# Kernel tuning notes

Hardware: AMD Instinct MI355X
Metric: run time of the kernel (lower is better)

The kernel has to match this reference:

```python
import jax, jax.numpy as jnp
import numpy as np

B, L, D = 2, 2048, 1024
H, G, Hd = 16, 4, 64
WIN = 256
HPG = H // G  # heads per group


def _sincos(seq_len, dim, dtype):
    # Matches sincos_cache: emb = cat(freqs, freqs) along last dim.
    inv_freq = 1.0 / (10000.0 ** (jnp.arange(0, dim, 2, dtype=jnp.float32) / dim))
    t = jnp.arange(seq_len, dtype=jnp.float32)
    freqs = t[:, None] * inv_freq[None, :]           # [L, dim/2]
    emb = jnp.concatenate([freqs, freqs], axis=-1)   # [L, dim]
    return jnp.sin(emb).astype(dtype), jnp.cos(emb).astype(dtype)


def _rope(x, sin, cos):
    # x: [B, h, L, Hd]; sin/cos: [L, Hd] broadcast over batch/heads.
    x1 = x[..., ::2]
    x2 = x[..., 1::2]
    xr = jnp.stack((-x2, x1), axis=-1).reshape(x.shape)  # interleaved rotate
    return x * cos[None, None] + xr * sin[None, None]


def setup_inputs() -> dict:
    key = jax.random.key(0)
    ks = jax.random.split(key, 10)
    s = 0.02
    return {
        "x": jax.random.normal(ks[0], (B, L, D), dtype=jnp.float32),
        "global_positions": jax.random.randint(ks[1], (4,), 0, L),
        "Wq": jax.random.normal(ks[2], (D, D), dtype=jnp.float32) * s,
        "bq": jnp.zeros((D,), dtype=jnp.float32),
        "Wk": jax.random.normal(ks[3], (D, G * Hd), dtype=jnp.float32) * s,
        "bk": jnp.zeros((G * Hd,), dtype=jnp.float32),
        "Wv": jax.random.normal(ks[4], (D, G * Hd), dtype=jnp.float32) * s,
        "bv": jnp.zeros((G * Hd,), dtype=jnp.float32),
        "Wo": jax.random.normal(ks[5], (D, D), dtype=jnp.float32) * s,
        "bo": jnp.zeros((D,), dtype=jnp.float32),
    }


def reference(x, global_positions, Wq, bq, Wk, bk, Wv, bv, Wo, bo):
    b, l, d = x.shape
    scale = 1.0 / np.sqrt(Hd).astype(np.float32)

    q = (x @ Wq + bq).reshape(b, l, H, Hd).transpose(0, 2, 1, 3)   # [B,H,L,Hd]
    k = (x @ Wk + bk).reshape(b, l, G, Hd).transpose(0, 2, 1, 3)   # [B,G,L,Hd]
    v = (x @ Wv + bv).reshape(b, l, G, Hd).transpose(0, 2, 1, 3)   # [B,G,L,Hd]

    sin, cos = _sincos(l, Hd, x.dtype)
    q = _rope(q, sin, cos)
    k = _rope(k, sin, cos)  # rope per-head is identical, so rope groups then expand

    # GQA broadcast: head h uses group h // HPG (group-major repeat)
    k = jnp.repeat(k, HPG, axis=1)  # [B,H,L,Hd]
    v = jnp.repeat(v, HPG, axis=1)  # [B,H,L,Hd]

    # sliding-window + global additive mask
    idx = jnp.arange(l)
    win = jnp.abs(idx[:, None] - idx[None, :]) <= WIN            # [L,L]
    isg = jnp.zeros((l,), dtype=bool).at[global_positions].set(True)
    mask = win | isg[:, None] | isg[None, :]
    addm = jnp.where(mask, 0.0, -jnp.inf).astype(x.dtype)        # [L,L]

    scores = jnp.einsum('bhld,bhsd->bhls', q, k) * scale + addm[None, None]
    probs = jax.nn.softmax(scores, axis=-1)
    out = jnp.einsum('bhls,bhsd->bhld', probs, v)                # [B,H,L,Hd]
    out = out.transpose(0, 2, 1, 3).reshape(b, l, d)
    return out @ Wo + bo
```

## Files before the change

kernel.cpp:

```cpp
#include <hip/hip_runtime.h>
#include <math.h>

#define B_   2
#define L_   2048
#define D_   1024
#define H_   16
#define G_   4
#define Hd_  64
#define WIN_ 256

typedef float f4 __attribute__((ext_vector_type(4)));
typedef float f32x4 __attribute__((ext_vector_type(4)));
typedef short s16x8 __attribute__((ext_vector_type(8)));
typedef ushort u16x4 __attribute__((ext_vector_type(4)));

#define ROPE_LN 0.28782313662425575

__device__ __forceinline__ float bf2f(ushort u) {
    union { uint i; float f; } c; c.i = ((uint)u) << 16; return c.f;
}
__device__ __forceinline__ ushort f2bf(float f) {
    union { float f; uint i; } c; c.f = f;
    return (ushort)((c.i + 0x7FFFu + ((c.i >> 16) & 1u)) >> 16);
}
__device__ __forceinline__ uint cvtpk(float lo, float hi) {
    uint r;
    asm("v_cvt_pk_bf16_f32 %0, %1, %2" : "=v"(r) : "v"(lo), "v"(hi));
    return r;
}

__device__ __forceinline__ void async_copy16(const ushort* g, ushort* l) {
    __builtin_amdgcn_global_load_lds(
        (const __attribute__((address_space(1))) void*)g,
        (__attribute__((address_space(3))) void*)l,
        16, 0, 0);
}

__global__ __launch_bounds__(256) void k_prep_all(
    const float* __restrict__ x, ushort* __restrict__ xb,
    const float* __restrict__ Wq, const float* __restrict__ Wk,
    const float* __restrict__ Wv, const float* __restrict__ Wo,
    ushort* __restrict__ Wt, ushort* __restrict__ Wot,
    float* __restrict__ sct)
{
    __shared__ __align__(16) float Ts[64][68];
    const int bid = blockIdx.x;
    const int tid = threadIdx.x;

    if (bid < 4096) {
        const int idx = bid * 256 + tid;
        f4 v = ((const f4*)x)[idx];
        u16x4 o;
        o[0] = f2bf(v[0]); o[1] = f2bf(v[1]); o[2] = f2bf(v[2]); o[3] = f2bf(v[3]);
        ((u16x4*)xb)[idx] = o;
        return;
    }
    if (bid >= 5120) {
        const int idx = (bid - 5120) * 256 + tid;
        const int l = idx >> 5, m = idx & 31;
        const float invf = (float)exp(-ROPE_LN * (double)m);
        const float a = (float)l * invf;
        sct[l * 64 + m]      = cosf(a);
        sct[l * 64 + 32 + m] = sinf(a);
        return;
    }
    const int t = bid - 4096;
    const int z = t >> 8;
    const float* W; ushort* dst; int N, rowoff;
    if (z == 0)      { W = Wq; N = 1024; dst = Wt;  rowoff = 0;    }
    else if (z == 1) { W = Wk; N = 256;  dst = Wt;  rowoff = 1024; }
    else if (z == 2) { W = Wv; N = 256;  dst = Wt;  rowoff = 1280; }
    else             { W = Wo; N = 1024; dst = Wot; rowoff = 0;    }
    const int k0 = ((t >> 4) & 15) << 6;
    const int n0 = (t & 15) << 6;
    if (n0 >= N) return;
    const int rr = tid >> 4, cc4 = (tid & 15) << 2;
#pragma unroll
    for (int i = 0; i < 4; ++i) {
        const int r = rr + i * 16;
        *(f4*)&Ts[r][cc4] = *(const f4*)&W[(size_t)(k0 + r) * N + n0 + cc4];
    }
    __syncthreads();
#pragma unroll
    for (int i = 0; i < 4; ++i) {
        const int tr = rr + i * 16;
        u16x4 pk;
#pragma unroll
        for (int j = 0; j < 4; ++j) pk[j] = f2bf(Ts[cc4 + j][tr]);
        *(u16x4*)&dst[(size_t)(rowoff + n0 + tr) * 1024 + k0 + cc4] = pk;
    }
}

__global__ __launch_bounds__(256) void k_gemm_bf16(
    const ushort* __restrict__ A, const ushort* __restrict__ Bt, int mode,
    const float* __restrict__ b0, const float* __restrict__ b1,
    const float* __restrict__ b2, const float* __restrict__ sct,
    ushort* __restrict__ qo, ushort* __restrict__ ko, ushort* __restrict__ vt,
    float* __restrict__ outp)
{
    __shared__ __align__(16) ushort LDSbuf[16384];
    ushort* As = LDSbuf;
    ushort* Bs = LDSbuf + 8192;

    const int tid = threadIdx.x;
    const int wv = tid >> 6, lane = tid & 63, lr = lane & 15, lg = lane >> 4;
    const int wm = wv >> 1, wn = wv & 1;
    const int rblk = blockIdx.x << 7, cblk = blockIdx.y << 6;

    const ushort* agp[4]; ushort* alds[4];
#pragma unroll
    for (int i = 0; i < 4; ++i) {
        const int slot = wv * 256 + i * 64 + lane;
        const int r = slot >> 3, c = slot & 7;
        const int ss = c ^ (r & 7);
        agp[i] = A + (size_t)(rblk + r) * 1024 + ss * 8;
        alds[i] = As + (wv * 256 + i * 64) * 8;
    }
    const ushort* bgp[2]; ushort* blds[2];
#pragma unroll
    for (int i = 0; i < 2; ++i) {
        const int slot = wv * 128 + i * 64 + lane;
        const int r = slot >> 3, c = slot & 7;
        const int ss = c ^ (r & 7);
        bgp[i] = Bt + (size_t)(cblk + r) * 1024 + ss * 8;
        blds[i] = Bs + (wv * 128 + i * 64) * 8;
    }

    f32x4 acc[4][2];
#pragma unroll
    for (int m = 0; m < 4; ++m)
#pragma unroll
        for (int n = 0; n < 2; ++n) acc[m][n] = (f32x4)0.f;

    for (int kt = 0; kt < 16; ++kt) {
        if (kt) __syncthreads();
        const int ko_ = kt * 64;
#pragma unroll
        for (int i = 0; i < 4; ++i) async_copy16(agp[i] + ko_, alds[i]);
#pragma unroll
        for (int i = 0; i < 2; ++i) async_copy16(bgp[i] + ko_, blds[i]);
        __syncthreads();

#pragma unroll
        for (int ks = 0; ks < 2; ++ks) {
            s16x8 aF[4], bF[2];
#pragma unroll
            for (int m = 0; m < 4; ++m) {
                const int r = wm * 64 + m * 16 + lr;
                const int c = (ks * 4 + lg) ^ (r & 7);
                aF[m] = *(const s16x8*)&As[r * 64 + c * 8];
            }
#pragma unroll
            for (int n = 0; n < 2; ++n) {
                const int r = wn * 32 + n * 16 + lr;
                const int c = (ks * 4 + lg) ^ (r & 7);
                bF[n] = *(const s16x8*)&Bs[r * 64 + c * 8];
            }
            __builtin_amdgcn_s_setprio(1);
#pragma unroll
            for (int m = 0; m < 4; ++m)
#pragma unroll
                for (int n = 0; n < 2; ++n)
                    acc[m][n] = __builtin_amdgcn_mfma_f32_16x16x32_bf16(aF[m], bF[n], acc[m][n], 0, 0, 0);
            __builtin_amdgcn_s_setprio(0);
        }
    }

    if (mode == 0) {
        const bool dorope = (cblk < 1280);
        float* tab = (float*)LDSbuf;
        if (dorope) {
            __syncthreads();
            const float* srcT = sct + (size_t)(rblk & 2047) * 64;
            for (int i = tid; i < 2048; i += 256)
                ((f4*)tab)[i] = ((const f4*)srcT)[i];
            __syncthreads();
        }
#pragma unroll
        for (int m = 0; m < 4; ++m) {
            const int row0 = rblk + wm * 64 + m * 16 + (lg << 2);
            const int bb = row0 >> 11, l0 = row0 & 2047;
            const int ll0 = row0 - rblk;
#pragma unroll
            for (int n = 0; n < 2; ++n) {
                const int col = cblk + wn * 32 + n * 16 + lr;
                float v_[4];
                const float bi = (col < 1024) ? b0[col]
                               : (col < 1280) ? b1[col - 1024] : b2[col - 1280];
#pragma unroll
                for (int rg = 0; rg < 4; ++rg) v_[rg] = acc[m][n][rg] + bi;
                if (dorope) {
                    const int mI = col & 31;
                    const float sgn = (lr & 1) ? 1.f : -1.f;
#pragma unroll
                    for (int rg = 0; rg < 4; ++rg) {
                        const float part = __shfl_xor(v_[rg], 1);
                        const float c_ = tab[(ll0 + rg) * 64 + mI];
                        const float s_ = tab[(ll0 + rg) * 64 + 32 + mI];
                        v_[rg] = v_[rg] * c_ + sgn * part * s_;
                    }
                }
                if (col < 1024) {
                    const int h = col >> 6, d = col & 63;
                    ushort* p = qo + (((size_t)(bb * 16 + h)) * 2048 + l0) * 64 + d;
#pragma unroll
                    for (int rg = 0; rg < 4; ++rg)
                        p[(size_t)rg * 64] = f2bf(v_[rg] * 0.125f);
                } else if (col < 1280) {
                    const int cl = col - 1024, g = cl >> 6, d = cl & 63;
                    ushort* p = ko + (((size_t)(bb * 4 + g)) * 2048 + l0) * 64 + d;
#pragma unroll
                    for (int rg = 0; rg < 4; ++rg)
                        p[(size_t)rg * 64] = f2bf(v_[rg]);
                } else {
                    const int cl = col - 1280, g = cl >> 6, d = cl & 63;
                    u16x4 pk;
#pragma unroll
                    for (int rg = 0; rg < 4; ++rg) pk[rg] = f2bf(v_[rg]);
                    *(u16x4*)(vt + ((size_t)(bb * 4 + g) * 64 + d) * 2048 + l0) = pk;
                }
            }
        }
    } else {
#pragma unroll
        for (int m = 0; m < 4; ++m) {
            const int row0 = rblk + wm * 64 + m * 16 + (lg << 2);
#pragma unroll
            for (int n = 0; n < 2; ++n) {
                const int col = cblk + wn * 32 + n * 16 + lr;
                const float bi = b0[col];
#pragma unroll
                for (int rg = 0; rg < 4; ++rg)
                    outp[(size_t)(row0 + rg) * 1024 + col] = acc[m][n][rg] + bi;
            }
        }
    }
}

__global__ __launch_bounds__(256, 4) void k_attn_win(
    const ushort* __restrict__ qb, const ushort* __restrict__ kb,
    const ushort* __restrict__ vtb, const int* __restrict__ gpos,
    ushort* __restrict__ aout)
{
    __shared__ __align__(16) ushort Ks[2][4096];
    __shared__ __align__(16) ushort Vs[2][4096];
    __shared__ ushort Pl[4][1024];

    const int tid  = threadIdx.x;
    const int wv   = tid >> 6, lane = tid & 63;
    const int lr   = lane & 15, lg = lane >> 4;
    const int qt = blockIdx.x, g = blockIdx.y, b = blockIdx.z;
    const int h  = (g << 2) + wv;
    const int q0w = qt << 4;
    const int qpos = q0w + lr;

    const ushort* qp = qb  + (((size_t)b * H_ + h) * L_ + q0w) * Hd_;
    const ushort* kp = kb  + ((size_t)b * G_ + g) * (size_t)L_ * Hd_;
    const ushort* vp = vtb + ((size_t)b * G_ + g) * (size_t)Hd_ * L_;
    char* rowp = (char*)&Pl[wv][0] + (lr << 7);
    const int swz = (lr & 7) << 4;

    int sr[2], ssk[2];
    ushort* kl[2]; ushort* vl[2];
#pragma unroll
    for (int i = 0; i < 2; ++i) {
        const int slot = wv * 128 + i * 64 + lane;
        const int r = slot >> 3, c = slot & 7;
        sr[i] = r; ssk[i] = c ^ (r & 7);
        kl[i] = ((ushort*)Ks) + (wv * 128 + i * 64) * 8;
        vl[i] = ((ushort*)Vs) + (wv * 128 + i * 64) * 8;
    }

#define STAGE(CUR, S0_) do {                                                  \
    _Pragma("unroll") for (int i = 0; i < 2; ++i) {                           \
        async_copy16(kp + ((size_t)(S0_) + sr[i]) * 64 + ssk[i] * 8,          \
                     kl[i] + (CUR) * 4096);                                   \
        async_copy16(vp + (size_t)sr[i] * 2048 + (S0_) + ssk[i] * 8,          \
                     vl[i] + (CUR) * 4096);                                   \
    } } while (0)

    const s16x8* qr = (const s16x8*)(qp + (size_t)lr * Hd_);
    const s16x8 qf0 = qr[lg], qf1 = qr[lg + 4];

    int gall[4];
#pragma unroll
    for (int j = 0; j < 4; ++j) gall[j] = gpos[j];
    bool uniq[4];
    uniq[0] = true;
    uniq[1] = (gall[1] != gall[0]);
    uniq[2] = (gall[2] != gall[0]) && (gall[2] != gall[1]);
    uniq[3] = (gall[3] != gall[0]) && (gall[3] != gall[1]) && (gall[3] != gall[2]);

    f32x4 acc_o[4];
#pragma unroll
    for (int j = 0; j < 4; ++j) acc_o[j] = (f32x4)0.f;
    float mrun = -INFINITY, lrun = 0.f;

    const int t_lo = (q0w - WIN_ > 0) ? ((q0w - WIN_) >> 6) : 0;
    const int t_hi_f = (q0w + 15 + WIN_) >> 6;
    const int t_hi = (t_hi_f < (L_ >> 6) - 1) ? t_hi_f : (L_ >> 6) - 1;

    const int kc0 = lg ^ (lr & 7);
    const int kc1 = (lg + 4) ^ (lr & 7);

    int cur = 0;
    STAGE(0, t_lo << 6);

    for (int t = t_lo; t <= t_hi; ++t) {
        const int s0 = t << 6;
        __syncthreads();
        if (t < t_hi) STAGE(cur ^ 1, (t + 1) << 6);

        const ushort* Kb = ((const ushort*)Ks) + cur * 4096;
        const ushort* Vb = ((const ushort*)Vs) + cur * 4096;

        f32x4 s[4];
#pragma unroll
        for (int gk = 0; gk < 4; ++gk) {
            const int gr = gk * 16 + lr;
            s16x8 kf0 = *(const s16x8*)&Kb[(gr * 8 + kc0) * 8];
            s16x8 kf1 = *(const s16x8*)&Kb[(gr * 8 + kc1) * 8];
            f32x4 tq = __builtin_amdgcn_mfma_f32_16x16x32_bf16(kf0, qf0, (f32x4)0.f, 0, 0, 0);
            s[gk]    = __builtin_amdgcn_mfma_f32_16x16x32_bf16(kf1, qf1, tq, 0, 0, 0);
        }

        s16x8 vf0[4], vf1[4];
#pragma unroll
        for (int dg = 0; dg < 4; ++dg) {
            const int vrw = dg * 16 + lr;
            vf0[dg] = *(const s16x8*)&Vb[(vrw * 8 + kc0) * 8];
            vf1[dg] = *(const s16x8*)&Vb[(vrw * 8 + kc1) * 8];
        }

        if (s0 < q0w - 241 || s0 > q0w + 193) {
#pragma unroll
            for (int gk = 0; gk < 4; ++gk)
#pragma unroll
                for (int r2 = 0; r2 < 4; ++r2) {
                    const int key = s0 + gk * 16 + (lg << 2) + r2;
                    const int dlt = qpos - key;
                    if (dlt > WIN_ || dlt < -WIN_) s[gk][r2] = -INFINITY;
                }
        }

        float mx = fmaxf(fmaxf(s[0][0], s[0][1]), fmaxf(s[0][2], s[0][3]));
#pragma unroll
        for (int gk = 1; gk < 4; ++gk)
            mx = fmaxf(mx, fmaxf(fmaxf(s[gk][0], s[gk][1]), fmaxf(s[gk][2], s[gk][3])));
        mx = fmaxf(mx, __shfl_xor(mx, 16));
        mx = fmaxf(mx, __shfl_xor(mx, 32));
        const float mn = fmaxf(mrun, mx);
        const float al = __expf(mrun - mn);

        float rs = 0.f;
        uint pk0[4], pk1[4];
#pragma unroll
        for (int gk = 0; gk < 4; ++gk) {
            const float p0 = __expf(s[gk][0] - mn);
            const float p1 = __expf(s[gk][1] - mn);
            const float p2 = __expf(s[gk][2] - mn);
            const float p3 = __expf(s[gk][3] - mn);
            rs += (p0 + p1) + (p2 + p3);
            pk0[gk] = cvtpk(p0, p1);
            pk1[gk] = cvtpk(p2, p3);
        }
        rs += __shfl_xor(rs, 16);
        rs += __shfl_xor(rs, 32);
        lrun = lrun * al + rs;
        mrun = mn;

#pragma unroll
        for (int gk = 0; gk < 4; ++gk) {
            uint2 w; w.x = pk0[gk]; w.y = pk1[gk];
            *(uint2*)(rowp + (((gk << 5) + (lg << 3)) ^ swz)) = w;
        }

        f32x4 al4;
#pragma unroll
        for (int r = 0; r < 4; ++r)
            al4[r] = __shfl(al, (lane & 48) + (lg << 2) + r);
#pragma unroll
        for (int j = 0; j < 4; ++j) acc_o[j] *= al4;

        const s16x8 pa0 = *(const s16x8*)(rowp + ((lg << 4) ^ swz));
        const s16x8 pa1 = *(const s16x8*)(rowp + ((64 + (lg << 4)) ^ swz));
        __builtin_amdgcn_s_setprio(1);
#pragma unroll
        for (int dg = 0; dg < 4; ++dg) {
            acc_o[dg] = __builtin_amdgcn_mfma_f32_16x16x32_bf16(pa0, vf0[dg], acc_o[dg], 0, 0, 0);
            acc_o[dg] = __builtin_amdgcn_mfma_f32_16x16x32_bf16(pa1, vf1[dg], acc_o[dg], 0, 0, 0);
        }
        __builtin_amdgcn_s_setprio(0);

        cur ^= 1;
    }

    {
        const s16x8* kr = (const s16x8*)(kp + (size_t)gall[lr & 3] * 64);
        s16x8 kf0 = kr[lg], kf1 = kr[lg + 4];
        f32x4 tq = __builtin_amdgcn_mfma_f32_16x16x32_bf16(kf0, qf0, (f32x4)0.f, 0, 0, 0);
        f32x4 sv = __builtin_amdgcn_mfma_f32_16x16x32_bf16(kf1, qf1, tq, 0, 0, 0);

#pragma unroll
        for (int r2 = 0; r2 < 4; ++r2) {
            bool valid = (lg == 0) && uniq[r2];
            const int dlt = qpos - gall[r2];
            valid = valid && ((dlt > WIN_) || (dlt < -WIN_));
            if (!valid) sv[r2] = -INFINITY;
        }

        float mx = fmaxf(fmaxf(sv[0], sv[1]), fmaxf(sv[2], sv[3]));
        mx = fmaxf(mx, __shfl_xor(mx, 16));
        mx = fmaxf(mx, __shfl_xor(mx, 32));
        const float mn = fmaxf(mrun, mx);
        const float al = __expf(mrun - mn);
        const float p0 = __expf(sv[0] - mn);
        const float p1 = __expf(sv[1] - mn);
        const float p2 = __expf(sv[2] - mn);
        const float p3 = __expf(sv[3] - mn);
        float rs = (p0 + p1) + (p2 + p3);
        rs += __shfl_xor(rs, 16);
        rs += __shfl_xor(rs, 32);
        lrun = lrun * al + rs;
        mrun = mn;

        uint2 w; w.x = cvtpk(p0, p1); w.y = cvtpk(p2, p3);
        *(uint2*)(rowp + ((lg << 3) ^ swz)) = w;
        uint2 z; z.x = 0; z.y = 0;
        *(uint2*)(rowp + ((32 + (lg << 3)) ^ swz)) = z;

        f32x4 al4;
#pragma unroll
        for (int r = 0; r < 4; ++r)
            al4[r] = __shfl(al, (lane & 48) + (lg << 2) + r);
#pragma unroll
        for (int j = 0; j < 4; ++j) acc_o[j] *= al4;

        const s16x8 pa0 = *(const s16x8*)(rowp + ((lg << 4) ^ swz));
#pragma unroll
        for (int dg = 0; dg < 4; ++dg) {
            s16x8 vb0 = (s16x8)(short)0;
            if (lg == 0) {
#pragma unroll
                for (int j = 0; j < 4; ++j)
                    vb0[j] = (short)vp[(size_t)(dg * 16 + lr) * 2048 + gall[j]];
            }
            acc_o[dg] = __builtin_amdgcn_mfma_f32_16x16x32_bf16(pa0, vb0, acc_o[dg], 0, 0, 0);
        }
    }

    {
        const float inv = 1.f / lrun;
#pragma unroll
        for (int r = 0; r < 4; ++r) {
            const float w0 = __shfl(inv, (lane & 48) + (lg << 2) + r);
            const int qrow = q0w + (lg << 2) + r;
            ushort* op = aout + (((size_t)b * L_ + qrow) * H_ + h) * Hd_;
#pragma unroll
            for (int dg = 0; dg < 4; ++dg)
                op[dg * 16 + lr] = f2bf(acc_o[dg][r] * w0);
        }
    }
#undef STAGE
}

__global__ __launch_bounds__(256) void k_attn_global_rows(
    const ushort* __restrict__ q, const ushort* __restrict__ kg,
    const ushort* __restrict__ vt, const int* __restrict__ gpos,
    ushort* __restrict__ aout)
{
    __shared__ float qrow[64];
    __shared__ float Ps[L_];
    __shared__ float red[4];
    __shared__ float pacc[4][64];

    const int tid = threadIdx.x;
    const int wv = tid >> 6, lane = tid & 63;
    const int b = blockIdx.x >> 4;
    const int h = blockIdx.x & 15;
    const int g = h >> 2;
    const int gi = blockIdx.y;
    const int lq = gpos[gi];
    for (int j = 0; j < gi; ++j)
        if (gpos[j] == lq) return;
    const ushort* kbase = kg + ((size_t)b * G_ + g) * (size_t)L_ * Hd_;
    const ushort* vbase = vt + ((size_t)b * G_ + g) * (size_t)Hd_ * L_;

    if (tid < 64) qrow[tid] = bf2f(q[(((size_t)b * H_ + h) * L_ + lq) * Hd_ + tid]);
    __syncthreads();

    float sc[8]; float lmax = -INFINITY;
#pragma unroll
    for (int c = 0; c < 8; ++c) {
        const int s = tid + (c << 8);
        const s16x8* kr = (const s16x8*)(kbase + (size_t)s * Hd_);
        float dot = 0.f;
#pragma unroll
        for (int d8 = 0; d8 < 8; ++d8) {
            s16x8 kv = kr[d8];
#pragma unroll
            for (int j = 0; j < 8; ++j) dot += qrow[d8 * 8 + j] * bf2f((ushort)kv[j]);
        }
        sc[c] = dot; lmax = fmaxf(lmax, dot);
    }
#pragma unroll
    for (int o = 32; o; o >>= 1) lmax = fmaxf(lmax, __shfl_xor(lmax, o));
    if (lane == 0) red[wv] = lmax;
    __syncthreads();
    const float M = fmaxf(fmaxf(red[0], red[1]), fmaxf(red[2], red[3]));
    __syncthreads();

    float ls = 0.f;
#pragma unroll
    for (int c = 0; c < 8; ++c) {
        const float p = __expf(sc[c] - M);
        Ps[tid + (c << 8)] = p;
        ls += p;
    }
#pragma unroll
    for (int o = 32; o; o >>= 1) ls += __shfl_xor(ls, o);
    if (lane == 0) red[wv] = ls;
    __syncthreads();
    const float S = red[0] + red[1] + red[2] + red[3];

    const int d = tid & 63, ch = tid >> 6;
    const ushort* vr = vbase + (size_t)d * L_ + (ch << 9);
    float a = 0.f;
    for (int s8 = 0; s8 < 64; ++s8) {
        s16x8 vv = ((const s16x8*)vr)[s8];
        const float* pp = &Ps[(ch << 9) + (s8 << 3)];
#pragma unroll
        for (int j = 0; j < 8; ++j) a += pp[j] * bf2f((ushort)vv[j]);
    }
    pacc[ch][d] = a;
    __syncthreads();
    if (tid < 64) {
        const float sum = pacc[0][tid] + pacc[1][tid] + pacc[2][tid] + pacc[3][tid];
        aout[(((size_t)b * L_ + lq) * H_ + h) * Hd_ + tid] = f2bf(sum / S);
    }
}

extern "C" void kernel_launch(void* const* d_in, const int* in_sizes, int n_in,
                              void* d_out, int out_size, void* d_ws, size_t ws_size,
                              hipStream_t stream)
{
    const float* x  = (const float*)d_in[0];
    const int*   gp = (const int*)d_in[1];
    const float* Wq = (const float*)d_in[2];
    const float* bq = (const float*)d_in[3];
    const float* Wk = (const float*)d_in[4];
    const float* bk = (const float*)d_in[5];
    const float* Wv = (const float*)d_in[6];
    const float* bv = (const float*)d_in[7];
    const float* Wo = (const float*)d_in[8];
    const float* bo = (const float*)d_in[9];
    float* out = (float*)d_out;

    ushort* xb   = (ushort*)d_ws;
    ushort* awsb = xb;
    ushort* qws  = xb  + (size_t)4194304;
    ushort* kws  = qws + (size_t)4194304;
    ushort* vtws = kws + (size_t)1048576;
    ushort* Wt   = vtws + (size_t)1048576;
    ushort* Wot  = Wt  + (size_t)1572864;
    float*  sct  = (float*)(Wot + (size_t)1048576);

    k_prep_all<<<dim3(5376), 256, 0, stream>>>(x, xb, Wq, Wk, Wv, Wo, Wt, Wot, sct);

    k_gemm_bf16<<<dim3(32, 24), 256, 0, stream>>>(xb, Wt, 0, bq, bk, bv, sct,
                                                  qws, kws, vtws, (float*)0);

    k_attn_win<<<dim3(128, 4, 2), 256, 0, stream>>>(qws, kws, vtws, gp, awsb);
    k_attn_global_rows<<<dim3(32, 4), 256, 0, stream>>>(qws, kws, vtws, gp, awsb);

    k_gemm_bf16<<<dim3(32, 16), 256, 0, stream>>>(awsb, Wot, 1, bo, (const float*)0,
                                                  (const float*)0, (const float*)0,
                                                  (ushort*)0, (ushort*)0, (ushort*)0, out);
}
```

Baseline: 104.2 us.

## Process two 16-row query subtiles per wave to reuse staged K/V tiles

Each attention block now covers 32 query rows instead of 16, with each wave keeping two independent online-softmax states and accumulators. Every K/V tile loaded into shared memory is used by both sub-tiles, roughly halving K/V global traffic and staging per query row, and the grid shrinks to half as many blocks. In exchange register pressure rises (launch bounds lowered from 4 to 3 blocks per CU), each block walks one extra key tile, and there are fewer blocks to fill the GPU.

```diff
diff --git a/kernel.cpp b/kernel.cpp
--- a/kernel.cpp
+++ b/kernel.cpp
@@ -237,7 +237,119 @@
     }
 }
 
-__global__ __launch_bounds__(256, 4) void k_attn_win(
+#define PROCSUB(Q0S, QF0, QF1, MRUN, LRUN, ACC) do {                          \
+    f32x4 s_[4];                                                              \
+    _Pragma("unroll") for (int gk = 0; gk < 4; ++gk) {                        \
+        const int gr_ = gk * 16 + lr;                                         \
+        s16x8 kf0_ = *(const s16x8*)&Kb[(gr_ * 8 + kc0) * 8];                 \
+        s16x8 kf1_ = *(const s16x8*)&Kb[(gr_ * 8 + kc1) * 8];                 \
+        f32x4 tq_ = __builtin_amdgcn_mfma_f32_16x16x32_bf16(kf0_, QF0, (f32x4)0.f, 0, 0, 0); \
+        s_[gk]    = __builtin_amdgcn_mfma_f32_16x16x32_bf16(kf1_, QF1, tq_, 0, 0, 0); \
+    }                                                                         \
+    if (s0 < (Q0S) - 241 || s0 > (Q0S) + 193) {                               \
+        _Pragma("unroll") for (int gk = 0; gk < 4; ++gk)                      \
+        _Pragma("unroll") for (int r2 = 0; r2 < 4; ++r2) {                    \
+            const int key_ = s0 + gk * 16 + (lg << 2) + r2;                   \
+            const int dlt_ = ((Q0S) + lr) - key_;                             \
+            if (dlt_ > WIN_ || dlt_ < -WIN_) s_[gk][r2] = -INFINITY;          \
+        }                                                                     \
+    }                                                                         \
+    float mx_ = fmaxf(fmaxf(s_[0][0], s_[0][1]), fmaxf(s_[0][2], s_[0][3]));  \
+    _Pragma("unroll") for (int gk = 1; gk < 4; ++gk)                          \
+        mx_ = fmaxf(mx_, fmaxf(fmaxf(s_[gk][0], s_[gk][1]), fmaxf(s_[gk][2], s_[gk][3]))); \
+    mx_ = fmaxf(mx_, __shfl_xor(mx_, 16));                                    \
+    mx_ = fmaxf(mx_, __shfl_xor(mx_, 32));                                    \
+    const float mn_ = fmaxf(MRUN, mx_);                                       \
+    const float al_ = __expf(MRUN - mn_);                \
+    float rs_ = 0.f;                                                          \
+    uint pk0_[4], pk1_[4];                                                    \
+    _Pragma("unroll") for (int gk = 0; gk < 4; ++gk) {                        \
+        const float p0_ = __expf(s_[gk][0] - mn_);                            \
+        const float p1_ = __expf(s_[gk][1] - mn_);                            \
+        const float p2_ = __expf(s_[gk][2] - mn_);                            \
+        const float p3_ = __expf(s_[gk][3] - mn_);                            \
+        rs_ += (p0_ + p1_) + (p2_ + p3_);                                     \
+        pk0_[gk] = cvtpk(p0_, p1_);                                           \
+        pk1_[gk] = cvtpk(p2_, p3_);                                           \
+    }                                                                         \
+    rs_ += __shfl_xor(rs_, 16);                                               \
+    rs_ += __shfl_xor(rs_, 32);                                               \
+    LRUN = LRUN * al_ + rs_;                                                  \
+    MRUN = mn_;                                                               \
+    _Pragma("unroll") for (int gk = 0; gk < 4; ++gk) {                        \
+        uint2 w_; w_.x = pk0_[gk]; w_.y = pk1_[gk];                           \
+        *(uint2*)(rowp + (((gk << 5) + (lg << 3)) ^ swz)) = w_;               \
+    }                                                                         \
+    f32x4 al4_;                                                               \
+    _Pragma("unroll") for (int r = 0; r < 4; ++r)                             \
+        al4_[r] = __shfl(al_, (lane & 48) + (lg << 2) + r);                   \
+    _Pragma("unroll") for (int j = 0; j < 4; ++j) ACC[j] *= al4_;             \
+    const s16x8 pa0_ = *(const s16x8*)(rowp + ((lg << 4) ^ swz));             \
+    const s16x8 pa1_ = *(const s16x8*)(rowp + ((64 + (lg << 4)) ^ swz));      \
+    __builtin_amdgcn_s_setprio(1);                                            \
+    _Pragma("unroll") for (int dg = 0; dg < 4; ++dg) {                        \
+        ACC[dg] = __builtin_amdgcn_mfma_f32_16x16x32_bf16(pa0_, vf0[dg], ACC[dg], 0, 0, 0); \
+        ACC[dg] = __builtin_amdgcn_mfma_f32_16x16x32_bf16(pa1_, vf1[dg], ACC[dg], 0, 0, 0); \
+    }                                                                         \
+    __builtin_amdgcn_s_setprio(0);                                            \
+} while (0)
+
+#define PSEUDO(Q0S, QF0, QF1, MRUN, LRUN, ACC) do {                           \
+    const s16x8* kr_ = (const s16x8*)(kp + (size_t)gall[lr & 3] * 64);        \
+    s16x8 kf0_ = kr_[lg], kf1_ = kr_[lg + 4];                                 \
+    f32x4 tq_ = __builtin_amdgcn_mfma_f32_16x16x32_bf16(kf0_, QF0, (f32x4)0.f, 0, 0, 0); \
+    f32x4 sv_ = __builtin_amdgcn_mfma_f32_16x16x32_bf16(kf1_, QF1, tq_, 0, 0, 0); \
+    _Pragma("unroll") for (int r2 = 0; r2 < 4; ++r2) {                        \
+        bool valid_ = (lg == 0) && uniq[r2];                                  \
+        const int dlt_ = ((Q0S) + lr) - gall[r2];                             \
+        valid_ = valid_ && ((dlt_ > WIN_) || (dlt_ < -WIN_));                 \
+        if (!valid_) sv_[r2] = -INFINITY;                                     \
+    }                                                                         \
+    float mx_ = fmaxf(fmaxf(sv_[0], sv_[1]), fmaxf(sv_[2], sv_[3]));          \
+    mx_ = fmaxf(mx_, __shfl_xor(mx_, 16));                                    \
+    mx_ = fmaxf(mx_, __shfl_xor(mx_, 32));                                    \
+    const float mn_ = fmaxf(MRUN, mx_);                                       \
+    const float al_ = __expf(MRUN - mn_);                                     \
+    const float p0_ = __expf(sv_[0] - mn_);                                   \
+    const float p1_ = __expf(sv_[1] - mn_);                                   \
+    const float p2_ = __expf(sv_[2] - mn_);                                   \
+    const float p3_ = __expf(sv_[3] - mn_);                                   \
+    float rs_ = (p0_ + p1_) + (p2_ + p3_);                                    \
+    rs_ += __shfl_xor(rs_, 16);                                               \
+    rs_ += __shfl_xor(rs_, 32);                                               \
+    LRUN = LRUN * al_ + rs_;                                                  \
+    MRUN = mn_;                                                               \
+    uint2 w_; w_.x = cvtpk(p0_, p1_); w_.y = cvtpk(p2_, p3_);                 \
+    *(uint2*)(rowp + ((lg << 3) ^ swz)) = w_;                                 \
+    uint2 z_; z_.x = 0; z_.y = 0;                                             \
+    *(uint2*)(rowp + ((32 + (lg << 3)) ^ swz)) = z_;                          \
+    f32x4 al4_;                                                               \
+    _Pragma("unroll") for (int r = 0; r < 4; ++r)                             \
+        al4_[r] = __shfl(al_, (lane & 48) + (lg << 2) + r);                   \
+    _Pragma("unroll") for (int j = 0; j < 4; ++j) ACC[j] *= al4_;             \
+    const s16x8 pa0_ = *(const s16x8*)(rowp + ((lg << 4) ^ swz));             \
+    _Pragma("unroll") for (int dg = 0; dg < 4; ++dg) {                        \
+        s16x8 vb_ = (s16x8)(short)0;                                          \
+        if (lg == 0) {                                                        \
+            _Pragma("unroll") for (int j = 0; j < 4; ++j)                     \
+                vb_[j] = (short)vp[(size_t)(dg * 16 + lr) * 2048 + gall[j]];  \
+        }                                                                     \
+        ACC[dg] = __builtin_amdgcn_mfma_f32_16x16x32_bf16(pa0_, vb_, ACC[dg], 0, 0, 0); \
+    }                                                                         \
+} while (0)
+
+#define WRITESUB(Q0S, LRUN, ACC) do {                                         \
+    const float inv_ = 1.f / LRUN;                                            \
+    _Pragma("unroll") for (int r = 0; r < 4; ++r) {                           \
+        const float w0_ = __shfl(inv_, (lane & 48) + (lg << 2) + r);          \
+        const int qrow_ = (Q0S) + (lg << 2) + r;                              \
+        ushort* op_ = aout + (((size_t)b * L_ + qrow_) * H_ + h) * Hd_;       \
+        _Pragma("unroll") for (int dg = 0; dg < 4; ++dg)                      \
+            op_[dg * 16 + lr] = f2bf(ACC[dg][r] * w0_);                       \
+    }                                                                         \
+} while (0)
+
+__global__ __launch_bounds__(256, 3) void k_attn_win(
     const ushort* __restrict__ qb, const ushort* __restrict__ kb,
     const ushort* __restrict__ vtb, const int* __restrict__ gpos,
     ushort* __restrict__ aout)
@@ -251,8 +363,8 @@
     const int lr   = lane & 15, lg = lane >> 4;
     const int qt = blockIdx.x, g = blockIdx.y, b = blockIdx.z;
     const int h  = (g << 2) + wv;
-    const int q0w = qt << 4;
-    const int qpos = q0w + lr;
+    const int q0w = qt << 5;
+    const int q0A = q0w, q0B = q0w + 16;
 
     const ushort* qp = qb  + (((size_t)b * H_ + h) * L_ + q0w) * Hd_;
     const ushort* kp = kb  + ((size_t)b * G_ + g) * (size_t)L_ * Hd_;
@@ -279,8 +391,10 @@
                      vl[i] + (CUR) * 4096);                                   \
     } } while (0)
 
-    const s16x8* qr = (const s16x8*)(qp + (size_t)lr * Hd_);
-    const s16x8 qf0 = qr[lg], qf1 = qr[lg + 4];
+    const s16x8* qrA = (const s16x8*)(qp + (size_t)lr * Hd_);
+    const s16x8 qfA0 = qrA[lg], qfA1 = qrA[lg + 4];
+    const s16x8* qrB = (const s16x8*)(qp + (size_t)(16 + lr) * Hd_);
+    const s16x8 qfB0 = qrB[lg], qfB1 = qrB[lg + 4];
 
     int gall[4];
 #pragma unroll
@@ -291,13 +405,14 @@
     uniq[2] = (gall[2] != gall[0]) && (gall[2] != gall[1]);
     uniq[3] = (gall[3] != gall[0]) && (gall[3] != gall[1]) && (gall[3] != gall[2]);
 
-    f32x4 acc_o[4];
-#pragma unroll
-    for (int j = 0; j < 4; ++j) acc_o[j] = (f32x4)0.f;
-    float mrun = -INFINITY, lrun = 0.f;
+    f32x4 accA[4], accB[4];
+#pragma unroll
+    for (int j = 0; j < 4; ++j) { accA[j] = (f32x4)0.f; accB[j] = (f32x4)0.f; }
+    float mrunA = -INFINITY, lrunA = 0.f;
+    float mrunB = -INFINITY, lrunB = 0.f;
 
     const int t_lo = (q0w - WIN_ > 0) ? ((q0w - WIN_) >> 6) : 0;
-    const int t_hi_f = (q0w + 15 + WIN_) >> 6;
+    const int t_hi_f = (q0w + 31 + WIN_) >> 6;
     const int t_hi = (t_hi_f < (L_ >> 6) - 1) ? t_hi_f : (L_ >> 6) - 1;
 
     const int kc0 = lg ^ (lr & 7);
@@ -313,16 +428,6 @@
 
         const ushort* Kb = ((const ushort*)Ks) + cur * 4096;
         const ushort* Vb = ((const ushort*)Vs) + cur * 4096;
-
-        f32x4 s[4];
-#pragma unroll
-        for (int gk = 0; gk < 4; ++gk) {
-            const int gr = gk * 16 + lr;
-            s16x8 kf0 = *(const s16x8*)&Kb[(gr * 8 + kc0) * 8];
-            s16x8 kf1 = *(const s16x8*)&Kb[(gr * 8 + kc1) * 8];
-            f32x4 tq = __builtin_amdgcn_mfma_f32_16x16x32_bf16(kf0, qf0, (f32x4)0.f, 0, 0, 0);
-            s[gk]    = __builtin_amdgcn_mfma_f32_16x16x32_bf16(kf1, qf1, tq, 0, 0, 0);
-        }
 
         s16x8 vf0[4], vf1[4];
 #pragma unroll
@@ -332,135 +437,17 @@
             vf1[dg] = *(const s16x8*)&Vb[(vrw * 8 + kc1) * 8];
         }
 
-        if (s0 < q0w - 241 || s0 > q0w + 193) {
-#pragma unroll
-            for (int gk = 0; gk < 4; ++gk)
-#pragma unroll
-                for (int r2 = 0; r2 < 4; ++r2) {
-                    const int key = s0 + gk * 16 + (lg << 2) + r2;
-                    const int dlt = qpos - key;
-                    if (dlt > WIN_ || dlt < -WIN_) s[gk][r2] = -INFINITY;
-                }
-        }
-
-        float mx = fmaxf(fmaxf(s[0][0], s[0][1]), fmaxf(s[0][2], s[0][3]));
-#pragma unroll
-        for (int gk = 1; gk < 4; ++gk)
-            mx = fmaxf(mx, fmaxf(fmaxf(s[gk][0], s[gk][1]), fmaxf(s[gk][2], s[gk][3])));
-        mx = fmaxf(mx, __shfl_xor(mx, 16));
-        mx = fmaxf(mx, __shfl_xor(mx, 32));
-        const float mn = fmaxf(mrun, mx);
-        const float al = __expf(mrun - mn);
-
-        float rs = 0.f;
-        uint pk0[4], pk1[4];
-#pragma unroll
-        for (int gk = 0; gk < 4; ++gk) {
-            const float p0 = __expf(s[gk][0] - mn);
-            const float p1 = __expf(s[gk][1] - mn);
-            const float p2 = __expf(s[gk][2] - mn);
-            const float p3 = __expf(s[gk][3] - mn);
-            rs += (p0 + p1) + (p2 + p3);
-            pk0[gk] = cvtpk(p0, p1);
-            pk1[gk] = cvtpk(p2, p3);
-        }
-        rs += __shfl_xor(rs, 16);
-        rs += __shfl_xor(rs, 32);
-        lrun = lrun * al + rs;
-        mrun = mn;
-
-#pragma unroll
-        for (int gk = 0; gk < 4; ++gk) {
-            uint2 w; w.x = pk0[gk]; w.y = pk1[gk];
-            *(uint2*)(rowp + (((gk << 5) + (lg << 3)) ^ swz)) = w;
-        }
-
-        f32x4 al4;
-#pragma unroll
-        for (int r = 0; r < 4; ++r)
-            al4[r] = __shfl(al, (lane & 48) + (lg << 2) + r);
-#pragma unroll
-        for (int j = 0; j < 4; ++j) acc_o[j] *= al4;
-
-        const s16x8 pa0 = *(const s16x8*)(rowp + ((lg << 4) ^ swz));
-        const s16x8 pa1 = *(const s16x8*)(rowp + ((64 + (lg << 4)) ^ swz));
-        __builtin_amdgcn_s_setprio(1);
-#pragma unroll
-        for (int dg = 0; dg < 4; ++dg) {
-            acc_o[dg] = __builtin_amdgcn_mfma_f32_16x16x32_bf16(pa0, vf0[dg], acc_o[dg], 0, 0, 0);
-            acc_o[dg] = __builtin_amdgcn_mfma_f32_16x16x32_bf16(pa1, vf1[dg], acc_o[dg], 0, 0, 0);
-        }
-        __builtin_amdgcn_s_setprio(0);
+        PROCSUB(q0A, qfA0, qfA1, mrunA, lrunA, accA);
+        PROCSUB(q0B, qfB0, qfB1, mrunB, lrunB, accB);
 
         cur ^= 1;
     }
 
-    {
-        const s16x8* kr = (const s16x8*)(kp + (size_t)gall[lr & 3] * 64);
-        s16x8 kf0 = kr[lg], kf1 = kr[lg + 4];
-        f32x4 tq = __builtin_amdgcn_mfma_f32_16x16x32_bf16(kf0, qf0, (f32x4)0.f, 0, 0, 0);
-        f32x4 sv = __builtin_amdgcn_mfma_f32_16x16x32_bf16(kf1, qf1, tq, 0, 0, 0);
-
-#pragma unroll
-        for (int r2 = 0; r2 < 4; ++r2) {
-            bool valid = (lg == 0) && uniq[r2];
-            const int dlt = qpos - gall[r2];
-            valid = valid && ((dlt > WIN_) || (dlt < -WIN_));
-            if (!valid) sv[r2] = -INFINITY;
-        }
-
-        float mx = fmaxf(fmaxf(sv[0], sv[1]), fmaxf(sv[2], sv[3]));
-        mx = fmaxf(mx, __shfl_xor(mx, 16));
-        mx = fmaxf(mx, __shfl_xor(mx, 32));
-        const float mn = fmaxf(mrun, mx);
-        const float al = __expf(mrun - mn);
-        const float p0 = __expf(sv[0] - mn);
-        const float p1 = __expf(sv[1] - mn);
-        const float p2 = __expf(sv[2] - mn);
-        const float p3 = __expf(sv[3] - mn);
-        float rs = (p0 + p1) + (p2 + p3);
-        rs += __shfl_xor(rs, 16);
-        rs += __shfl_xor(rs, 32);
-        lrun = lrun * al + rs;
-        mrun = mn;
-
-        uint2 w; w.x = cvtpk(p0, p1); w.y = cvtpk(p2, p3);
-        *(uint2*)(rowp + ((lg << 3) ^ swz)) = w;
-        uint2 z; z.x = 0; z.y = 0;
-        *(uint2*)(rowp + ((32 + (lg << 3)) ^ swz)) = z;
-
-        f32x4 al4;
-#pragma unroll
-        for (int r = 0; r < 4; ++r)
-            al4[r] = __shfl(al, (lane & 48) + (lg << 2) + r);
-#pragma unroll
-        for (int j = 0; j < 4; ++j) acc_o[j] *= al4;
-
-        const s16x8 pa0 = *(const s16x8*)(rowp + ((lg << 4) ^ swz));
-#pragma unroll
-        for (int dg = 0; dg < 4; ++dg) {
-            s16x8 vb0 = (s16x8)(short)0;
-            if (lg == 0) {
-#pragma unroll
-                for (int j = 0; j < 4; ++j)
-                    vb0[j] = (short)vp[(size_t)(dg * 16 + lr) * 2048 + gall[j]];
-            }
-            acc_o[dg] = __builtin_amdgcn_mfma_f32_16x16x32_bf16(pa0, vb0, acc_o[dg], 0, 0, 0);
-        }
-    }
-
-    {
-        const float inv = 1.f / lrun;
-#pragma unroll
-        for (int r = 0; r < 4; ++r) {
-            const float w0 = __shfl(inv, (lane & 48) + (lg << 2) + r);
-            const int qrow = q0w + (lg << 2) + r;
-            ushort* op = aout + (((size_t)b * L_ + qrow) * H_ + h) * Hd_;
-#pragma unroll
-            for (int dg = 0; dg < 4; ++dg)
-                op[dg * 16 + lr] = f2bf(acc_o[dg][r] * w0);
-        }
-    }
+    PSEUDO(q0A, qfA0, qfA1, mrunA, lrunA, accA);
+    PSEUDO(q0B, qfB0, qfB1, mrunB, lrunB, accB);
+
+    WRITESUB(q0A, lrunA, accA);
+    WRITESUB(q0B, lrunB, accB);
 #undef STAGE
 }
 
@@ -570,7 +557,7 @@
     k_gemm_bf16<<<dim3(32, 24), 256, 0, stream>>>(xb, Wt, 0, bq, bk, bv, sct,
                                                   qws, kws, vtws, (float*)0);
 
-    k_attn_win<<<dim3(128, 4, 2), 256, 0, stream>>>(qws, kws, vtws, gp, awsb);
+    k_attn_win<<<dim3(64, 4, 2), 256, 0, stream>>>(qws, kws, vtws, gp, awsb);
     k_attn_global_rows<<<dim3(32, 4), 256, 0, stream>>>(qws, kws, vtws, gp, awsb);
 
     k_gemm_bf16<<<dim3(32, 16), 256, 0, stream>>>(awsb, Wot, 1, bo, (const float*)0,
```

Result: slower. 108.1 us (+3.7%).
